# Kernel optimization log

Measured on AMD Instinct MI355X. Metric: run time of the kernel, lower is better.

Reference implementation:

```python
import jax, jax.numpy as jnp
import numpy as np

# KroneckerLinear: W ~= sum_i (A_i kron B_i); efficient path computes, per token,
# Y = sum_i A_i @ X @ B_i^T with X = x.reshape(in1, in2), output flattened as (out1*out2).

IN1, IN2 = 64, 64      # in_factors (in1*in2 = in_features = 4096)
OUT1, OUT2 = 64, 64    # out_factors (out1*out2 = out_features = 4096)
NUM_SUM = 2
BATCH, SEQ = 4, 4096


def setup_inputs() -> dict:
    key = jax.random.key(0)
    kx, ka, kb, kbias = jax.random.split(key, 4)
    x = jax.random.normal(kx, (BATCH, SEQ, IN1 * IN2), dtype=jnp.float32)
    # kaiming-uniform-like scale for small factors
    bound_a = 1.0 / np.sqrt(IN1)
    bound_b = 1.0 / np.sqrt(IN2)
    A = jax.random.uniform(ka, (NUM_SUM, OUT1, IN1), dtype=jnp.float32, minval=-bound_a, maxval=bound_a)
    B = jax.random.uniform(kb, (NUM_SUM, OUT2, IN2), dtype=jnp.float32, minval=-bound_b, maxval=bound_b)
    bound = 1.0 / np.sqrt(IN1 * IN2)
    bias = jax.random.uniform(kbias, (OUT1 * OUT2,), dtype=jnp.float32, minval=-bound, maxval=bound)
    return {"x": x, "A": A, "B": B, "bias": bias}


def reference(x, A, B, bias):
    Bsz, T, _ = x.shape
    X = x.reshape(Bsz, T, IN1, IN2)  # (b, t, i, j)
    # y[b,t,o,p] = sum_s sum_ij A[s,o,i] * X[b,t,i,j] * B[s,p,j]  -> (out1, out2)
    y = jnp.einsum("btij,soi,spj->btop", X, A, B)
    return y.reshape(Bsz, T, OUT1 * OUT2) + bias
```

## Files before the change

### kernel.cpp

```cpp
#include <hip/hip_runtime.h>
#include <hip/hip_bf16.h>

typedef float  f32x4  __attribute__((ext_vector_type(4)));
typedef short  bf16x8 __attribute__((ext_vector_type(8)));

#define NT      16384
#define NBLOCK  512
#define TPS     (NT / NBLOCK)

#define WAITV(n) asm volatile("s_waitcnt vmcnt(" #n ")" ::: "memory")

__device__ __forceinline__ short f2bf(float x) {
  return (short)__builtin_bit_cast(unsigned short, __float2bfloat16(x));
}

__device__ __forceinline__ void gload16(const float* gp, float* lp) {
  __builtin_amdgcn_global_load_lds((const __attribute__((address_space(1))) void*)gp,
                                   (__attribute__((address_space(3))) void*)lp,
                                   16, 0, 0);
}

__device__ __forceinline__ unsigned ldsaddr(const void* p) {
  return (unsigned)(uintptr_t)(const __attribute__((address_space(3))) void*)p;
}

__device__ __forceinline__ void stage(float* XB, const float* gbase, int lane) {
#pragma unroll
  for (int q = 0; q < 16; ++q) {
    const int i = q * 4 + (lane >> 4);
    const float* gp = gbase + i * 64 + (((lane & 15) ^ (i & 7)) << 2);
    gload16(gp, XB + q * 256);
  }
}

__global__ __launch_bounds__(64, 1)
void kron_kernel(const float* __restrict__ x,
                 const float* __restrict__ A,
                 const float* __restrict__ Bm,
                 const float* __restrict__ bias,
                 float* __restrict__ out) {
  __shared__ float  xh[3][4096];
  __shared__ bf16x8 AT[1024];
  __shared__ bf16x8 BT[1024];

  const int lane = threadIdx.x;
  const int g    = lane >> 4;
  const int l15  = lane & 15;
  const int bid  = blockIdx.x;

  for (int idx = 0; idx < 16; ++idx) {
    const int s = idx >> 3, ot = (idx & 7) >> 1, c = idx & 1;
    const int o = ot * 16 + l15;
    bf16x8 v;
#pragma unroll
    for (int e = 0; e < 8; ++e) {
      const int i = c * 32 + 4 * g + (e & 3) + 16 * (e >> 2);
      v[e] = f2bf(A[s * 4096 + o * 64 + i]);
    }
    AT[idx * 64 + lane] = v;
  }
  for (int idx = 0; idx < 16; ++idx) {
    const int s = idx >> 3, pt = (idx & 7) >> 1, jc = idx & 1;
    const int p = pt * 16 + l15;
    bf16x8 v;
#pragma unroll
    for (int e = 0; e < 8; ++e)
      v[e] = f2bf(Bm[s * 4096 + p * 64 + (jc * 32 + 8 * g + e)]);
    BT[idx * 64 + lane] = v;
  }

  const int pcol = 4 * g;
  f32x4 bv[4][4];
#pragma unroll
  for (int pt = 0; pt < 4; ++pt)
#pragma unroll
    for (int ot = 0; ot < 4; ++ot)
      bv[pt][ot] = *(const f32x4*)(bias + (ot * 16 + l15) * 64 + pt * 16 + pcol);

  float* b0 = &xh[0][0];
  float* b1 = &xh[1][0];
  float* b2 = &xh[2][0];
  stage(b0, x + ((size_t)bid << 12), lane);
  stage(b1, x + ((size_t)(bid + NBLOCK) << 12), lane);

  for (int k = 0; k < TPS; ++k) {
    if (k == 0)                    WAITV(16);
    else if (k == 1 || k == TPS-1) WAITV(32);
    else                           WAITV(48);

    if (k + 2 < TPS)
      stage(b2, x + ((size_t)(bid + (k + 2) * NBLOCK) << 12), lane);

    const unsigned ba = ldsaddr(b0);
    f32x4 r0[4][2], r1[4][2];
#pragma unroll
    for (int it = 0; it < 4; ++it) {
      const unsigned base = ba + (unsigned)(it * 16 + l15) * 256u;
      const unsigned m    = (unsigned)(l15 & 7);
#pragma unroll
      for (int jc = 0; jc < 2; ++jc) {
        const unsigned c0 = (unsigned)(8 * jc + 2 * g);
        asm volatile("ds_read_b128 %0, %1" : "=v"(r0[it][jc]) : "v"(base + ((c0 ^ m) << 4)) : "memory");
        asm volatile("ds_read_b128 %0, %1" : "=v"(r1[it][jc]) : "v"(base + (((c0 + 1u) ^ m) << 4)) : "memory");
      }
    }
    asm volatile("s_waitcnt lgkmcnt(0)" ::: "memory");
    __builtin_amdgcn_sched_barrier(0);

    bf16x8 xf[4][2];
#pragma unroll
    for (int it = 0; it < 4; ++it)
#pragma unroll
      for (int jc = 0; jc < 2; ++jc) {
        bf16x8 t;
        t[0]=f2bf(r0[it][jc][0]); t[1]=f2bf(r0[it][jc][1]);
        t[2]=f2bf(r0[it][jc][2]); t[3]=f2bf(r0[it][jc][3]);
        t[4]=f2bf(r1[it][jc][0]); t[5]=f2bf(r1[it][jc][1]);
        t[6]=f2bf(r1[it][jc][2]); t[7]=f2bf(r1[it][jc][3]);
        xf[it][jc] = t;
      }

    f32x4 acc2[4][4];
#pragma unroll
    for (int pt = 0; pt < 4; ++pt)
#pragma unroll
      for (int ot = 0; ot < 4; ++ot)
        acc2[pt][ot] = bv[pt][ot];

#pragma unroll
    for (int s = 0; s < 2; ++s) {
      bf16x8 bfr[4][2];
#pragma unroll
      for (int pt = 0; pt < 4; ++pt)
#pragma unroll
        for (int jc = 0; jc < 2; ++jc)
          bfr[pt][jc] = BT[(s * 8 + pt * 2 + jc) * 64 + lane];

      f32x4 a1[4][4];
#pragma unroll
      for (int a = 0; a < 4; ++a)
#pragma unroll
        for (int b = 0; b < 4; ++b)
          a1[a][b] = (f32x4){0.f, 0.f, 0.f, 0.f};
#pragma unroll
      for (int it = 0; it < 4; ++it)
#pragma unroll
        for (int pt = 0; pt < 4; ++pt)
#pragma unroll
          for (int jc = 0; jc < 2; ++jc)
            a1[it][pt] = __builtin_amdgcn_mfma_f32_16x16x32_bf16(
                xf[it][jc], bfr[pt][jc], a1[it][pt], 0, 0, 0);

      bf16x8 uf[4][2];
#pragma unroll
      for (int pt = 0; pt < 4; ++pt)
#pragma unroll
        for (int c = 0; c < 2; ++c) {
          bf16x8 t;
#pragma unroll
          for (int e = 0; e < 8; ++e)
            t[e] = f2bf(a1[(e >> 2) + 2 * c][pt][e & 3]);
          uf[pt][c] = t;
        }

      bf16x8 afr[4][2];
#pragma unroll
      for (int ot = 0; ot < 4; ++ot)
#pragma unroll
        for (int c = 0; c < 2; ++c)
          afr[ot][c] = AT[(s * 8 + ot * 2 + c) * 64 + lane];

#pragma unroll
      for (int pt = 0; pt < 4; ++pt)
#pragma unroll
        for (int ot = 0; ot < 4; ++ot)
#pragma unroll
          for (int c = 0; c < 2; ++c)
            acc2[pt][ot] = __builtin_amdgcn_mfma_f32_16x16x32_bf16(
                uf[pt][c], afr[ot][c], acc2[pt][ot], 0, 0, 0);
    }

    float* ob = out + (((size_t)(k * NBLOCK + bid)) << 12);
#pragma unroll
    for (int pt = 0; pt < 4; ++pt)
#pragma unroll
      for (int ot = 0; ot < 4; ++ot)
        *(f32x4*)(ob + (ot * 16 + l15) * 64 + pt * 16 + pcol) = acc2[pt][ot];

    float* t = b0; b0 = b1; b1 = b2; b2 = t;
  }
}

extern "C" void kernel_launch(void* const* d_in, const int* in_sizes, int n_in,
                              void* d_out, int out_size, void* d_ws, size_t ws_size,
                              hipStream_t stream) {
  const float* x    = (const float*)d_in[0];
  const float* A    = (const float*)d_in[1];
  const float* B    = (const float*)d_in[2];
  const float* bias = (const float*)d_in[3];
  float* out        = (float*)d_out;
  kron_kernel<<<dim3(NBLOCK), dim3(64), 0, stream>>>(x, A, B, bias, out);
}
```

Before: 105.2 us.

## Pack four independent token-stream waves per block with double-buffered LDS staging

Grid changes from 512 single-wave blocks to 256 blocks of 4 waves, each wave processing its own token stream. The four waves split the A/B bf16 transposition into LDS and synchronise once. Each wave's staging drops from triple to double buffering, and the next tile is issued into the just-read buffer right after its LDS reads complete. The aim is to share the setup cost and raise per-CU occupancy for latency hiding. The cost is a shallower prefetch per wave, and the vmcnt thresholds carried over from the triple-buffer scheme may no longer match the new load pattern.

```diff
diff --git a/kernel.cpp b/kernel.cpp
--- a/kernel.cpp
+++ b/kernel.cpp
@@ -5,10 +5,10 @@
 typedef short  bf16x8 __attribute__((ext_vector_type(8)));
 
 #define NT      16384
-#define NBLOCK  512
-#define TPS     (NT / NBLOCK)
-
-#define WAITV(n) asm volatile("s_waitcnt vmcnt(" #n ")" ::: "memory")
+#define NBLOCK  256
+#define WPB     4
+#define NSTREAM (NBLOCK * WPB)
+#define TPS     (NT / NSTREAM)
 
 __device__ __forceinline__ short f2bf(float x) {
   return (short)__builtin_bit_cast(unsigned short, __float2bfloat16(x));
@@ -33,22 +33,26 @@
   }
 }
 
-__global__ __launch_bounds__(64, 1)
+__global__ __launch_bounds__(256, 1)
 void kron_kernel(const float* __restrict__ x,
                  const float* __restrict__ A,
                  const float* __restrict__ Bm,
                  const float* __restrict__ bias,
                  float* __restrict__ out) {
-  __shared__ float  xh[3][4096];
+  __shared__ float  xh[WPB][2][4096];
   __shared__ bf16x8 AT[1024];
   __shared__ bf16x8 BT[1024];
 
-  const int lane = threadIdx.x;
+  const int tid  = threadIdx.x;
+  const int lane = tid & 63;
+  const int w    = tid >> 6;
   const int g    = lane >> 4;
   const int l15  = lane & 15;
-  const int bid  = blockIdx.x;
-
-  for (int idx = 0; idx < 16; ++idx) {
+  const int sid  = blockIdx.x * WPB + w;
+
+#pragma unroll
+  for (int t = 0; t < 4; ++t) {
+    const int idx = w * 4 + t;
     const int s = idx >> 3, ot = (idx & 7) >> 1, c = idx & 1;
     const int o = ot * 16 + l15;
     bf16x8 v;
@@ -59,7 +63,9 @@
     }
     AT[idx * 64 + lane] = v;
   }
-  for (int idx = 0; idx < 16; ++idx) {
+#pragma unroll
+  for (int t = 0; t < 4; ++t) {
+    const int idx = w * 4 + t;
     const int s = idx >> 3, pt = (idx & 7) >> 1, jc = idx & 1;
     const int p = pt * 16 + l15;
     bf16x8 v;
@@ -77,21 +83,20 @@
     for (int ot = 0; ot < 4; ++ot)
       bv[pt][ot] = *(const f32x4*)(bias + (ot * 16 + l15) * 64 + pt * 16 + pcol);
 
-  float* b0 = &xh[0][0];
-  float* b1 = &xh[1][0];
-  float* b2 = &xh[2][0];
-  stage(b0, x + ((size_t)bid << 12), lane);
-  stage(b1, x + ((size_t)(bid + NBLOCK) << 12), lane);
+  __syncthreads();
+
+  float* b0 = &xh[w][0][0];
+  float* b1 = &xh[w][1][0];
+
+  stage(b0, x + ((size_t)sid << 12), lane);
+  stage(b1, x + ((size_t)(sid + NSTREAM) << 12), lane);
 
   for (int k = 0; k < TPS; ++k) {
-    if (k == 0)                    WAITV(16);
-    else if (k == 1 || k == TPS-1) WAITV(32);
-    else                           WAITV(48);
-
-    if (k + 2 < TPS)
-      stage(b2, x + ((size_t)(bid + (k + 2) * NBLOCK) << 12), lane);
-
-    const unsigned ba = ldsaddr(b0);
+    if (k == 0)                        asm volatile("s_waitcnt vmcnt(16)" ::: "memory");
+    else if (k == 1 || k == TPS - 1)   asm volatile("s_waitcnt vmcnt(32)" ::: "memory");
+    else                               asm volatile("s_waitcnt vmcnt(48)" ::: "memory");
+
+    const unsigned ba = ldsaddr((k & 1) ? b1 : b0);
     f32x4 r0[4][2], r1[4][2];
 #pragma unroll
     for (int it = 0; it < 4; ++it) {
@@ -107,6 +112,10 @@
     asm volatile("s_waitcnt lgkmcnt(0)" ::: "memory");
     __builtin_amdgcn_sched_barrier(0);
 
+    if (k + 2 < TPS)
+      stage((k & 1) ? b1 : b0,
+            x + ((size_t)((k + 2) * NSTREAM + sid) << 12), lane);
+
     bf16x8 xf[4][2];
 #pragma unroll
     for (int it = 0; it < 4; ++it)
@@ -180,14 +189,12 @@
                 uf[pt][c], afr[ot][c], acc2[pt][ot], 0, 0, 0);
     }
 
-    float* ob = out + (((size_t)(k * NBLOCK + bid)) << 12);
-#pragma unroll
-    for (int pt = 0; pt < 4; ++pt)
-#pragma unroll
-      for (int ot = 0; ot < 4; ++ot)
+    float* ob = out + (((size_t)(k * NSTREAM + sid)) << 12);
+#pragma unroll
+    for (int ot = 0; ot < 4; ++ot)
+#pragma unroll
+      for (int pt = 0; pt < 4; ++pt)
         *(f32x4*)(ob + (ot * 16 + l15) * 64 + pt * 16 + pcol) = acc2[pt][ot];
-
-    float* t = b0; b0 = b1; b1 = b2; b2 = t;
   }
 }
 
@@ -199,5 +206,5 @@
   const float* B    = (const float*)d_in[2];
   const float* bias = (const float*)d_in[3];
   float* out        = (float*)d_out;
-  kron_kernel<<<dim3(NBLOCK), dim3(64), 0, stream>>>(x, A, B, bias, out);
-}
+  kron_kernel<<<dim3(NBLOCK), dim3(256), 0, stream>>>(x, A, B, bias, out);
+}
```

New measurement: 114.0 us. 1.08x slower.
